# Kernel optimization log

Hardware: AMD Instinct MI355X
Metric: run time of the kernel (lower is better)

## Reference

```python
import jax, jax.numpy as jnp
import numpy as np

N = 50000   # nodes
E = 800000  # edges per edge type
H = 4       # attention heads
C = 64      # per-head out channels
EPS = 1e-5  # batchnorm eps


def gat_conv(x, ei, W, a_s, a_d, b):
    # PyG GATConv with add_self_loops=True, concat=True, negative_slope=0.2
    h = (x @ W).reshape(-1, H, C)                      # [N,H,C]
    sl = jnp.arange(N)
    src = jnp.concatenate([ei[0], sl])                 # [E+N]
    dst = jnp.concatenate([ei[1], sl])
    al_s = (h * a_s).sum(-1)                           # [N,H]
    al_d = (h * a_d).sum(-1)
    e = jax.nn.leaky_relu(al_s[src] + al_d[dst], 0.2)  # [E+N,H]
    m = jax.ops.segment_max(e, dst, num_segments=N)    # segment softmax over dst
    ex = jnp.exp(e - m[dst])
    s = jax.ops.segment_sum(ex, dst, num_segments=N)
    alpha = ex / (s[dst] + 1e-16)                      # [E+N,H]
    out = jax.ops.segment_sum(alpha[:, :, None] * h[src], dst, num_segments=N)
    return out.reshape(N, H * C) + b


def bn(x, g, b):
    mu = x.mean(0)
    v = jnp.var(x, 0)
    return g * (x - mu) * jax.lax.rsqrt(v + EPS) + b


def setup_inputs() -> dict:
    key = jax.random.key(0)
    ks = jax.random.split(key, 20)
    p = {}
    p["x"] = jax.random.normal(ks[0], (N, 128), jnp.float32)
    p["edge_index_spatial"] = jax.random.randint(ks[1], (2, E), 0, N)
    p["edge_index_temporal"] = jax.random.randint(ks[2], (2, E), 0, N)
    ins = [128, 256, 256, 256]
    k = 3
    for i in range(4):
        sc = 1.0 / np.sqrt(ins[i]).astype(np.float32)
        p[f"W{i+1}"] = jax.random.normal(ks[k], (ins[i], H * C), jnp.float32) * sc; k += 1
        p[f"as{i+1}"] = jax.random.normal(ks[k], (H, C), jnp.float32) * 0.1; k += 1
        p[f"ad{i+1}"] = jax.random.normal(ks[k], (H, C), jnp.float32) * 0.1; k += 1
        p[f"b{i+1}"] = jnp.zeros((H * C,), jnp.float32)
        p[f"g{i+1}"] = jnp.ones((H * C,), jnp.float32)
        p[f"be{i+1}"] = jnp.zeros((H * C,), jnp.float32)
    p["Wl"] = jax.random.normal(ks[k], (H * C, 32), jnp.float32) * (1.0 / 16.0)
    p["bl"] = jnp.zeros((32,), jnp.float32)
    return p


def reference(x, edge_index_spatial, edge_index_temporal,
              W1, as1, ad1, b1, g1, be1,
              W2, as2, ad2, b2, g2, be2,
              W3, as3, ad3, b3, g3, be3,
              W4, as4, ad4, b4, g4, be4,
              Wl, bl):
    h = jax.nn.relu(bn(gat_conv(x, edge_index_spatial, W1, as1, ad1, b1), g1, be1))
    h = jax.nn.relu(bn(gat_conv(h, edge_index_spatial, W2, as2, ad2, b2), g2, be2))
    h = jax.nn.relu(bn(gat_conv(h, edge_index_temporal, W3, as3, ad3, b3), g3, be3))
    h = jax.nn.relu(bn(gat_conv(h, edge_index_temporal, W4, as4, ad4, b4), g4, be4))
    return h @ Wl + bl
```

## Files before the change

### kernel.cpp

```cpp
#include <hip/hip_runtime.h>
#include <hip/hip_bf16.h>
#include <hip/hip_fp16.h>
#include <math.h>

#define N_NODES 50000
#define N_EDGES 800000
#define NH 4
#define HC 256
#define TOT_E (N_EDGES + N_NODES)
#define SCAN_NB ((N_NODES + 255) / 256)

static __device__ __forceinline__ float lrelu(float x) { return x >= 0.f ? x : 0.2f * x; }

__global__ __launch_bounds__(256) void count_kernel(const int* __restrict__ ei,
                                                    int* __restrict__ cnt) {
    int i = blockIdx.x * blockDim.x + threadIdx.x;
    if (i >= TOT_E) return;
    int dst = (i < N_EDGES) ? ei[N_EDGES + i] : (i - N_EDGES);
    atomicAdd(&cnt[dst], 1);
}

__global__ __launch_bounds__(256) void scan1_kernel(const int* __restrict__ cnt,
                                                    int* __restrict__ offs,
                                                    int* __restrict__ bsum) {
    __shared__ int sm[256];
    const int t = threadIdx.x;
    const int base = blockIdx.x * 256;
    int v = (base + t < N_NODES) ? cnt[base + t] : 0;
    sm[t] = v;
    __syncthreads();
#pragma unroll
    for (int d = 1; d < 256; d <<= 1) {
        int add = (t >= d) ? sm[t - d] : 0;
        __syncthreads();
        sm[t] += add;
        __syncthreads();
    }
    if (base + t < N_NODES) offs[base + t] = sm[t] - v;
    if (t == 255) bsum[blockIdx.x] = sm[255];
}

__global__ __launch_bounds__(256) void scan2_kernel(int* __restrict__ bsum,
                                                    int* __restrict__ total) {
    __shared__ int sm[256];
    const int t = threadIdx.x;
    int v = (t < SCAN_NB) ? bsum[t] : 0;
    sm[t] = v;
    __syncthreads();
#pragma unroll
    for (int d = 1; d < 256; d <<= 1) {
        int add = (t >= d) ? sm[t - d] : 0;
        __syncthreads();
        sm[t] += add;
        __syncthreads();
    }
    if (t < SCAN_NB) bsum[t] = sm[t] - v;
    if (t == 255) *total = sm[255];
}

__global__ __launch_bounds__(256) void scan3_kernel(int* __restrict__ offs,
                                                    const int* __restrict__ bsum) {
    int i = blockIdx.x * blockDim.x + threadIdx.x;
    if (i < N_NODES) offs[i] += bsum[i >> 8];
}

__global__ __launch_bounds__(256) void scatter_kernel(const int* __restrict__ ei,
                                                      const int* __restrict__ offs,
                                                      int* __restrict__ cursor,
                                                      int* __restrict__ ssrc) {
    int i = blockIdx.x * blockDim.x + threadIdx.x;
    if (i >= TOT_E) return;
    int src, dst;
    if (i < N_EDGES) { src = ei[i]; dst = ei[N_EDGES + i]; }
    else             { src = i - N_EDGES; dst = src; }
    int pos = offs[dst] + atomicAdd(&cursor[dst], 1);
    ssrc[pos] = src;
}

__global__ __launch_bounds__(256) void gemm_kernel(const float* __restrict__ A,
                                                   const float* __restrict__ B,
                                                   __half* __restrict__ C,
                                                   const float* __restrict__ bnscale,
                                                   const float* __restrict__ bnshift,
                                                   const float* __restrict__ a_s,
                                                   const float* __restrict__ a_d,
                                                   float* __restrict__ als,
                                                   float* __restrict__ ald,
                                                   int M, int K) {
    __shared__ float As[16][128];
    __shared__ float Bs[16][128];
    const int t = threadIdx.x;
    const int tx = t & 15, ty = t >> 4;
    const int bm = blockIdx.x * 128;
    const int bn = blockIdx.y * 128;
    const int ar = t >> 2;
    const int ak = (t & 3) << 2;
    const int bk = t >> 5;
    const int bn4 = (t & 31) << 2;
    float acc[8][8] = {{0.f}};
    for (int k0 = 0; k0 < K; k0 += 16) {
        float4 sc = make_float4(1.f, 1.f, 1.f, 1.f);
        float4 sh = make_float4(0.f, 0.f, 0.f, 0.f);
        if (bnscale) {
            sc = *(const float4*)(bnscale + k0 + ak);
            sh = *(const float4*)(bnshift + k0 + ak);
        }
#pragma unroll
        for (int r = 0; r < 2; ++r) {
            int row = bm + r * 64 + ar;
            float4 a4 = make_float4(0.f, 0.f, 0.f, 0.f);
            if (row < M) a4 = *(const float4*)(A + (size_t)row * K + k0 + ak);
            if (bnscale) {
                a4.x = fmaxf(0.f, fmaf(a4.x, sc.x, sh.x));
                a4.y = fmaxf(0.f, fmaf(a4.y, sc.y, sh.y));
                a4.z = fmaxf(0.f, fmaf(a4.z, sc.z, sh.z));
                a4.w = fmaxf(0.f, fmaf(a4.w, sc.w, sh.w));
            }
            As[ak + 0][r * 64 + ar] = a4.x;
            As[ak + 1][r * 64 + ar] = a4.y;
            As[ak + 2][r * 64 + ar] = a4.z;
            As[ak + 3][r * 64 + ar] = a4.w;
        }
#pragma unroll
        for (int r = 0; r < 2; ++r) {
            int kk = r * 8 + bk;
            *(float4*)&Bs[kk][bn4] = *(const float4*)(B + (size_t)(k0 + kk) * HC + bn + bn4);
        }
        __syncthreads();
#pragma unroll
        for (int kk = 0; kk < 16; ++kk) {
            float a[8], b[8];
            *(float4*)&a[0] = *(const float4*)&As[kk][ty * 8];
            *(float4*)&a[4] = *(const float4*)&As[kk][ty * 8 + 4];
            *(float4*)&b[0] = *(const float4*)&Bs[kk][tx * 8];
            *(float4*)&b[4] = *(const float4*)&Bs[kk][tx * 8 + 4];
#pragma unroll
            for (int i = 0; i < 8; ++i)
#pragma unroll
                for (int j = 0; j < 8; ++j)
                    acc[i][j] = fmaf(a[i], b[j], acc[i][j]);
        }
        __syncthreads();
    }
#pragma unroll
    for (int i = 0; i < 8; ++i) {
        int row = bm + ty * 8 + i;
        if (row < M) {
            __half hv[8];
#pragma unroll
            for (int j = 0; j < 8; ++j) hv[j] = __float2half(acc[i][j]);
            *(uint4*)(C + (size_t)row * HC + bn + tx * 8) = *(uint4*)hv;
        }
    }
    const int ch0 = bn + tx * 8;
    float asv[8], adv[8];
#pragma unroll
    for (int j = 0; j < 8; ++j) { asv[j] = a_s[ch0 + j]; adv[j] = a_d[ch0 + j]; }
#pragma unroll
    for (int i = 0; i < 8; ++i) {
        int row = bm + ty * 8 + i;
        float ps = 0.f, pd = 0.f;
#pragma unroll
        for (int j = 0; j < 8; ++j) {
            ps = fmaf(acc[i][j], asv[j], ps);
            pd = fmaf(acc[i][j], adv[j], pd);
        }
#pragma unroll
        for (int d = 1; d < 8; d <<= 1) {
            ps += __shfl_xor(ps, d, 64);
            pd += __shfl_xor(pd, d, 64);
        }
        if ((tx & 7) == 0 && row < M) {
            int head = (bn >> 6) + (tx >> 3);
            als[row * NH + head] = ps;
            ald[row * NH + head] = pd;
        }
    }
}

__global__ __launch_bounds__(256) void gat_edge_kernel(const __half* __restrict__ h,
                                                       const int* __restrict__ offs,
                                                       const int* __restrict__ ssrc,
                                                       const float* __restrict__ als,
                                                       const float* __restrict__ ald,
                                                       const float* __restrict__ bias,
                                                       float* __restrict__ out) {
    __shared__ float ex_sm[4][64][NH];
    __shared__ int   src_sm[4][64];
    const int lane = threadIdx.x & 63;
    const int w = threadIdx.x >> 6;
    const int v = (blockIdx.x << 2) + w;
    if (v >= N_NODES) return;
    const int hh = lane >> 4;
    const float4 aldv4 = *(const float4*)(ald + v * NH);
    const int beg = offs[v], end = offs[v + 1];

    float4 m4 = make_float4(-INFINITY, -INFINITY, -INFINITY, -INFINITY);
    float4 s4 = make_float4(0.f, 0.f, 0.f, 0.f);
    float ax = 0.f, ay = 0.f, az = 0.f, aw = 0.f;

    for (int c0 = beg; c0 < end; c0 += 64) {
        const int n = min(64, end - c0);
        const int s0 = ssrc[c0];
        int srcl = s0;
        float4 e4 = make_float4(-INFINITY, -INFINITY, -INFINITY, -INFINITY);
        if (lane < n) {
            srcl = ssrc[c0 + lane];
            float4 a4 = *(const float4*)(als + srcl * NH);
            e4.x = lrelu(a4.x + aldv4.x);
            e4.y = lrelu(a4.y + aldv4.y);
            e4.z = lrelu(a4.z + aldv4.z);
            e4.w = lrelu(a4.w + aldv4.w);
        }
        float4 cm = e4;
#pragma unroll
        for (int d = 1; d < 64; d <<= 1) {
            cm.x = fmaxf(cm.x, __shfl_xor(cm.x, d, 64));
            cm.y = fmaxf(cm.y, __shfl_xor(cm.y, d, 64));
            cm.z = fmaxf(cm.z, __shfl_xor(cm.z, d, 64));
            cm.w = fmaxf(cm.w, __shfl_xor(cm.w, d, 64));
        }
        const float4 mn = make_float4(fmaxf(m4.x, cm.x), fmaxf(m4.y, cm.y),
                                      fmaxf(m4.z, cm.z), fmaxf(m4.w, cm.w));
        const float4 r4 = make_float4(__expf(m4.x - mn.x), __expf(m4.y - mn.y),
                                      __expf(m4.z - mn.z), __expf(m4.w - mn.w));
        float4 ex4;
        ex4.x = __expf(e4.x - mn.x);
        ex4.y = __expf(e4.y - mn.y);
        ex4.z = __expf(e4.z - mn.z);
        ex4.w = __expf(e4.w - mn.w);
        src_sm[w][lane] = srcl;
        *(float4*)&ex_sm[w][lane][0] = ex4;
        float4 se = ex4;
#pragma unroll
        for (int d = 1; d < 64; d <<= 1) {
            se.x += __shfl_xor(se.x, d, 64);
            se.y += __shfl_xor(se.y, d, 64);
            se.z += __shfl_xor(se.z, d, 64);
            se.w += __shfl_xor(se.w, d, 64);
        }
        s4 = make_float4(fmaf(s4.x, r4.x, se.x), fmaf(s4.y, r4.y, se.y),
                         fmaf(s4.z, r4.z, se.z), fmaf(s4.w, r4.w, se.w));
        const float rh = hh == 0 ? r4.x : hh == 1 ? r4.y : hh == 2 ? r4.z : r4.w;
        ax *= rh; ay *= rh; az *= rh; aw *= rh;
        m4 = mn;

        const int trip = (n + 7) & ~7;
        int sj[8]; float wj[8];
#pragma unroll
        for (int q = 0; q < 8; ++q) { sj[q] = src_sm[w][q]; wj[q] = ex_sm[w][q][hh]; }
        const int co = lane << 2;
        for (int j = 0; j < trip; j += 8) {
            uint2 raw[8];
#pragma unroll
            for (int q = 0; q < 8; ++q)
                raw[q] = *(const uint2*)(h + (size_t)sj[q] * HC + co);
            float u[8];
#pragma unroll
            for (int q = 0; q < 8; ++q) u[q] = wj[q];
            if (j + 8 < trip) {
#pragma unroll
                for (int q = 0; q < 8; ++q) {
                    sj[q] = src_sm[w][j + 8 + q];
                    wj[q] = ex_sm[w][j + 8 + q][hh];
                }
            }
#pragma unroll
            for (int q = 0; q < 8; ++q) {
                const __half2 lo = *reinterpret_cast<const __half2*>(&raw[q].x);
                const __half2 hi = *reinterpret_cast<const __half2*>(&raw[q].y);
                const float2 f0 = __half22float2(lo);
                const float2 f1 = __half22float2(hi);
                ax = fmaf(u[q], f0.x, ax); ay = fmaf(u[q], f0.y, ay);
                az = fmaf(u[q], f1.x, az); aw = fmaf(u[q], f1.y, aw);
            }
        }
    }

    const float sh = hh == 0 ? s4.x : hh == 1 ? s4.y : hh == 2 ? s4.z : s4.w;
    const float inv = 1.f / (sh + 1e-16f);
    const float4 b4 = *(const float4*)(bias + (lane << 2));
    *(float4*)(out + (size_t)v * HC + (lane << 2)) =
        make_float4(fmaf(ax, inv, b4.x), fmaf(ay, inv, b4.y),
                    fmaf(az, inv, b4.z), fmaf(aw, inv, b4.w));
}

__global__ __launch_bounds__(256) void bn_stats_kernel(const float* __restrict__ y,
                                                       double* __restrict__ sum,
                                                       double* __restrict__ sqsum) {
    const int t = threadIdx.x;
    const int r0 = blockIdx.x * 128;
    const int r1 = min(r0 + 128, N_NODES);
    float s = 0.f, q = 0.f;
    for (int r = r0; r < r1; ++r) {
        float v = y[(size_t)r * HC + t];
        s += v;
        q = fmaf(v, v, q);
    }
    atomicAdd(&sum[t], (double)s);
    atomicAdd(&sqsum[t], (double)q);
}

__global__ void bn_finalize_kernel(const double* __restrict__ sum,
                                   const double* __restrict__ sqsum,
                                   const float* __restrict__ g,
                                   const float* __restrict__ be,
                                   float* __restrict__ scale,
                                   float* __restrict__ shift) {
    int t = threadIdx.x;
    double mean = sum[t] / (double)N_NODES;
    double var = sqsum[t] / (double)N_NODES - mean * mean;
    float sc = g[t] * rsqrtf((float)var + 1e-5f);
    scale[t] = sc;
    shift[t] = be[t] - (float)mean * sc;
}

__global__ __launch_bounds__(256) void linear_kernel(const float* __restrict__ y,
                                                     const float* __restrict__ Wl,
                                                     const float* __restrict__ bl,
                                                     const float* __restrict__ scale,
                                                     const float* __restrict__ shift,
                                                     float* __restrict__ out) {
    __shared__ float Wls[256 * 32];
    __shared__ float scs[256], shs[256];
    const int t = threadIdx.x;
    for (int i = t; i < 256 * 32; i += 256) Wls[i] = Wl[i];
    scs[t] = scale[t];
    shs[t] = shift[t];
    __syncthreads();
    int gid = blockIdx.x * 256 + t;
    if (gid >= N_NODES * 32) return;
    int n = gid >> 5, j = gid & 31;
    float acc = bl[j];
    const float4* yrow = (const float4*)(y + (size_t)n * HC);
#pragma unroll
    for (int k4 = 0; k4 < 64; ++k4) {
        float4 y4 = yrow[k4];
        int k = k4 << 2;
        y4.x = fmaxf(0.f, fmaf(y4.x, scs[k + 0], shs[k + 0]));
        y4.y = fmaxf(0.f, fmaf(y4.y, scs[k + 1], shs[k + 1]));
        y4.z = fmaxf(0.f, fmaf(y4.z, scs[k + 2], shs[k + 2]));
        y4.w = fmaxf(0.f, fmaf(y4.w, scs[k + 3], shs[k + 3]));
        acc = fmaf(y4.x, Wls[(k + 0) * 32 + j], acc);
        acc = fmaf(y4.y, Wls[(k + 1) * 32 + j], acc);
        acc = fmaf(y4.z, Wls[(k + 2) * 32 + j], acc);
        acc = fmaf(y4.w, Wls[(k + 3) * 32 + j], acc);
    }
    out[gid] = acc;
}

extern "C" void kernel_launch(void* const* d_in, const int* in_sizes, int n_in,
                              void* d_out, int out_size, void* d_ws, size_t ws_size,
                              hipStream_t stream) {
    const float* x     = (const float*)d_in[0];
    const int* ei_sp   = (const int*)d_in[1];
    const int* ei_tp   = (const int*)d_in[2];
    const float* Wl    = (const float*)d_in[27];
    const float* bl    = (const float*)d_in[28];

    char* ws = (char*)d_ws;
    size_t off = 0;
    auto alloc = [&](size_t bytes) -> char* {
        char* p = ws + off;
        off = (off + bytes + 255) & ~(size_t)255;
        return p;
    };
    __half* buf0   = (__half*)alloc((size_t)N_NODES * HC * 2);
    float* buf1    = (float*)alloc((size_t)N_NODES * HC * 4);
    float* als     = (float*)alloc((size_t)N_NODES * NH * 4);
    float* ald     = (float*)alloc((size_t)N_NODES * NH * 4);
    int*   offs_sp = (int*)alloc((size_t)(N_NODES + 1) * 4);
    int*   offs_tp = (int*)alloc((size_t)(N_NODES + 1) * 4);
    int*   src_sp  = (int*)alloc((size_t)TOT_E * 4);
    int*   src_tp  = (int*)alloc((size_t)TOT_E * 4);
    int*   cnt     = (int*)alloc((size_t)N_NODES * 4);
    int*   bsum    = (int*)alloc((size_t)SCAN_NB * 4);
    double* bnsum  = (double*)alloc(256 * 8 * 2);
    double* bnsq   = bnsum + 256;
    float* scale   = (float*)alloc(256 * 4);
    float* shift   = (float*)alloc(256 * 4);
    (void)ws_size; (void)in_sizes; (void)n_in; (void)out_size;

    const int EB = (TOT_E + 255) / 256;

    hipMemsetAsync(cnt, 0, (size_t)N_NODES * 4, stream);
    count_kernel<<<EB, 256, 0, stream>>>(ei_sp, cnt);
    scan1_kernel<<<SCAN_NB, 256, 0, stream>>>(cnt, offs_sp, bsum);
    scan2_kernel<<<1, 256, 0, stream>>>(bsum, offs_sp + N_NODES);
    scan3_kernel<<<SCAN_NB, 256, 0, stream>>>(offs_sp, bsum);
    hipMemsetAsync(cnt, 0, (size_t)N_NODES * 4, stream);
    scatter_kernel<<<EB, 256, 0, stream>>>(ei_sp, offs_sp, cnt, src_sp);

    hipMemsetAsync(cnt, 0, (size_t)N_NODES * 4, stream);
    count_kernel<<<EB, 256, 0, stream>>>(ei_tp, cnt);
    scan1_kernel<<<SCAN_NB, 256, 0, stream>>>(cnt, offs_tp, bsum);
    scan2_kernel<<<1, 256, 0, stream>>>(bsum, offs_tp + N_NODES);
    scan3_kernel<<<SCAN_NB, 256, 0, stream>>>(offs_tp, bsum);
    hipMemsetAsync(cnt, 0, (size_t)N_NODES * 4, stream);
    scatter_kernel<<<EB, 256, 0, stream>>>(ei_tp, offs_tp, cnt, src_tp);

    const int NB4 = (N_NODES + 3) / 4;
    const dim3 ggrid((N_NODES + 127) / 128, 2);
    for (int L = 0; L < 4; ++L) {
        const float* in = (L == 0) ? x : buf1;
        const int K = (L == 0) ? 128 : 256;
        const float* bns = (L == 0) ? nullptr : scale;
        const float* bnh = (L == 0) ? nullptr : shift;
        const int* offs = (L < 2) ? offs_sp : offs_tp;
        const int* ssrc = (L < 2) ? src_sp : src_tp;
        const int base = 3 + L * 6;
        const float* W  = (const float*)d_in[base + 0];
        const float* as_ = (const float*)d_in[base + 1];
        const float* ad_ = (const float*)d_in[base + 2];
        const float* b_  = (const float*)d_in[base + 3];
        const float* g_  = (const float*)d_in[base + 4];
        const float* be_ = (const float*)d_in[base + 5];

        gemm_kernel<<<ggrid, 256, 0, stream>>>(in, W, buf0, bns, bnh,
                                               as_, ad_, als, ald, N_NODES, K);
        gat_edge_kernel<<<NB4, 256, 0, stream>>>(buf0, offs, ssrc, als, ald, b_, buf1);

        hipMemsetAsync(bnsum, 0, 256 * 8 * 2, stream);
        bn_stats_kernel<<<(N_NODES + 127) / 128, 256, 0, stream>>>(buf1, bnsum, bnsq);
        bn_finalize_kernel<<<1, 256, 0, stream>>>(bnsum, bnsq, g_, be_, scale, shift);
    }

    linear_kernel<<<(N_NODES * 32 + 255) / 256, 256, 0, stream>>>(buf1, Wl, bl,
                                                                  scale, shift,
                                                                  (float*)d_out);
}
```

Before: 1.178 ms.

## Use split-bf16 MFMA matrix cores for the node feature GEMM

Replaces the FP32 scalar-FMA tiled GEMM with an MFMA 16x16x32 bf16 implementation. Each fp32 input is split into high and low bf16 parts, and three MFMAs per tile (hi*hi, hi*lo, lo*hi) recover near-fp32 accuracy. The shared-memory layout changes to k-contiguous bf16 tiles, and the attention-logit epilogue is reworked for the MFMA output layout. This adds conversion work and makes the fp16 output stores scalar and strided in exchange for much higher matrix throughput.

```diff
diff --git a/kernel.cpp b/kernel.cpp
--- a/kernel.cpp
+++ b/kernel.cpp
@@ -10,7 +10,16 @@
 #define TOT_E (N_EDGES + N_NODES)
 #define SCAN_NB ((N_NODES + 255) / 256)
 
+typedef __attribute__((ext_vector_type(8))) short short8;
+typedef __attribute__((ext_vector_type(4))) float f32x4;
+
 static __device__ __forceinline__ float lrelu(float x) { return x >= 0.f ? x : 0.2f * x; }
+
+static __device__ __forceinline__ unsigned short bf16_rne(float x) {
+    unsigned int u = __float_as_uint(x);
+    u += 0x7fff + ((u >> 16) & 1);
+    return (unsigned short)(u >> 16);
+}
 
 __global__ __launch_bounds__(256) void count_kernel(const int* __restrict__ ei,
                                                     int* __restrict__ cnt) {
@@ -87,93 +96,135 @@
                                                    float* __restrict__ als,
                                                    float* __restrict__ ald,
                                                    int M, int K) {
-    __shared__ float As[16][128];
-    __shared__ float Bs[16][128];
+    __shared__ unsigned short Ah[128][40], Al[128][40];
+    __shared__ unsigned short Bh[128][40], Bl[128][40];
     const int t = threadIdx.x;
-    const int tx = t & 15, ty = t >> 4;
+    const int l = t & 63;
+    const int w = t >> 6;
+    const int wr = w >> 1, wc = w & 1;
+    const int fr = l & 15;
+    const int kg = (l >> 4) << 3;
     const int bm = blockIdx.x * 128;
     const int bn = blockIdx.y * 128;
-    const int ar = t >> 2;
-    const int ak = (t & 3) << 2;
-    const int bk = t >> 5;
-    const int bn4 = (t & 31) << 2;
-    float acc[8][8] = {{0.f}};
-    for (int k0 = 0; k0 < K; k0 += 16) {
-        float4 sc = make_float4(1.f, 1.f, 1.f, 1.f);
-        float4 sh = make_float4(0.f, 0.f, 0.f, 0.f);
-        if (bnscale) {
-            sc = *(const float4*)(bnscale + k0 + ak);
-            sh = *(const float4*)(bnshift + k0 + ak);
-        }
-#pragma unroll
-        for (int r = 0; r < 2; ++r) {
-            int row = bm + r * 64 + ar;
-            float4 a4 = make_float4(0.f, 0.f, 0.f, 0.f);
-            if (row < M) a4 = *(const float4*)(A + (size_t)row * K + k0 + ak);
-            if (bnscale) {
-                a4.x = fmaxf(0.f, fmaf(a4.x, sc.x, sh.x));
-                a4.y = fmaxf(0.f, fmaf(a4.y, sc.y, sh.y));
-                a4.z = fmaxf(0.f, fmaf(a4.z, sc.z, sh.z));
-                a4.w = fmaxf(0.f, fmaf(a4.w, sc.w, sh.w));
-            }
-            As[ak + 0][r * 64 + ar] = a4.x;
-            As[ak + 1][r * 64 + ar] = a4.y;
-            As[ak + 2][r * 64 + ar] = a4.z;
-            As[ak + 3][r * 64 + ar] = a4.w;
-        }
-#pragma unroll
-        for (int r = 0; r < 2; ++r) {
-            int kk = r * 8 + bk;
-            *(float4*)&Bs[kk][bn4] = *(const float4*)(B + (size_t)(k0 + kk) * HC + bn + bn4);
-        }
-        __syncthreads();
-#pragma unroll
-        for (int kk = 0; kk < 16; ++kk) {
-            float a[8], b[8];
-            *(float4*)&a[0] = *(const float4*)&As[kk][ty * 8];
-            *(float4*)&a[4] = *(const float4*)&As[kk][ty * 8 + 4];
-            *(float4*)&b[0] = *(const float4*)&Bs[kk][tx * 8];
-            *(float4*)&b[4] = *(const float4*)&Bs[kk][tx * 8 + 4];
-#pragma unroll
-            for (int i = 0; i < 8; ++i)
-#pragma unroll
-                for (int j = 0; j < 8; ++j)
-                    acc[i][j] = fmaf(a[i], b[j], acc[i][j]);
-        }
-        __syncthreads();
-    }
-#pragma unroll
-    for (int i = 0; i < 8; ++i) {
-        int row = bm + ty * 8 + i;
-        if (row < M) {
-            __half hv[8];
-#pragma unroll
-            for (int j = 0; j < 8; ++j) hv[j] = __float2half(acc[i][j]);
-            *(uint4*)(C + (size_t)row * HC + bn + tx * 8) = *(uint4*)hv;
-        }
-    }
-    const int ch0 = bn + tx * 8;
-    float asv[8], adv[8];
-#pragma unroll
-    for (int j = 0; j < 8; ++j) { asv[j] = a_s[ch0 + j]; adv[j] = a_d[ch0 + j]; }
-#pragma unroll
-    for (int i = 0; i < 8; ++i) {
-        int row = bm + ty * 8 + i;
-        float ps = 0.f, pd = 0.f;
-#pragma unroll
-        for (int j = 0; j < 8; ++j) {
-            ps = fmaf(acc[i][j], asv[j], ps);
-            pd = fmaf(acc[i][j], adv[j], pd);
-        }
-#pragma unroll
-        for (int d = 1; d < 8; d <<= 1) {
-            ps += __shfl_xor(ps, d, 64);
-            pd += __shfl_xor(pd, d, 64);
-        }
-        if ((tx & 7) == 0 && row < M) {
-            int head = (bn >> 6) + (tx >> 3);
-            als[row * NH + head] = ps;
-            ald[row * NH + head] = pd;
+    const int ra = t >> 1, ka = (t & 1) << 4;
+    const int nb = (t & 31) << 2, kb = (t >> 5) << 2;
+
+    f32x4 acc[4][4] = {};
+
+    for (int k0 = 0; k0 < K; k0 += 32) {
+        {
+            const int row = bm + ra;
+#pragma unroll
+            for (int i = 0; i < 4; ++i) {
+                const int kk = ka + 4 * i;
+                float4 a4 = make_float4(0.f, 0.f, 0.f, 0.f);
+                if (row < M) a4 = *(const float4*)(A + (size_t)row * K + k0 + kk);
+                if (bnscale) {
+                    float4 sc = *(const float4*)(bnscale + k0 + kk);
+                    float4 sh = *(const float4*)(bnshift + k0 + kk);
+                    a4.x = fmaxf(0.f, fmaf(a4.x, sc.x, sh.x));
+                    a4.y = fmaxf(0.f, fmaf(a4.y, sc.y, sh.y));
+                    a4.z = fmaxf(0.f, fmaf(a4.z, sc.z, sh.z));
+                    a4.w = fmaxf(0.f, fmaf(a4.w, sc.w, sh.w));
+                }
+                unsigned short h[4], lo[4];
+                float v[4] = {a4.x, a4.y, a4.z, a4.w};
+#pragma unroll
+                for (int q = 0; q < 4; ++q) {
+                    h[q] = bf16_rne(v[q]);
+                    float hf = __uint_as_float((unsigned int)h[q] << 16);
+                    lo[q] = bf16_rne(v[q] - hf);
+                }
+                *(uint2*)&Ah[ra][kk] = *(uint2*)h;
+                *(uint2*)&Al[ra][kk] = *(uint2*)lo;
+            }
+        }
+        {
+            float4 bv[4];
+#pragma unroll
+            for (int i = 0; i < 4; ++i)
+                bv[i] = *(const float4*)(B + (size_t)(k0 + kb + i) * HC + bn + nb);
+#pragma unroll
+            for (int c = 0; c < 4; ++c) {
+                float v[4] = {c == 0 ? bv[0].x : c == 1 ? bv[0].y : c == 2 ? bv[0].z : bv[0].w,
+                              c == 0 ? bv[1].x : c == 1 ? bv[1].y : c == 2 ? bv[1].z : bv[1].w,
+                              c == 0 ? bv[2].x : c == 1 ? bv[2].y : c == 2 ? bv[2].z : bv[2].w,
+                              c == 0 ? bv[3].x : c == 1 ? bv[3].y : c == 2 ? bv[3].z : bv[3].w};
+                unsigned short h[4], lo[4];
+#pragma unroll
+                for (int q = 0; q < 4; ++q) {
+                    h[q] = bf16_rne(v[q]);
+                    float hf = __uint_as_float((unsigned int)h[q] << 16);
+                    lo[q] = bf16_rne(v[q] - hf);
+                }
+                *(uint2*)&Bh[nb + c][kb] = *(uint2*)h;
+                *(uint2*)&Bl[nb + c][kb] = *(uint2*)lo;
+            }
+        }
+        __syncthreads();
+        short8 ahf[4], alf[4], bhf[4], blf[4];
+#pragma unroll
+        for (int m = 0; m < 4; ++m) {
+            ahf[m] = *(const short8*)&Ah[wr * 64 + m * 16 + fr][kg];
+            alf[m] = *(const short8*)&Al[wr * 64 + m * 16 + fr][kg];
+        }
+#pragma unroll
+        for (int n = 0; n < 4; ++n) {
+            bhf[n] = *(const short8*)&Bh[wc * 64 + n * 16 + fr][kg];
+            blf[n] = *(const short8*)&Bl[wc * 64 + n * 16 + fr][kg];
+        }
+#pragma unroll
+        for (int m = 0; m < 4; ++m)
+#pragma unroll
+            for (int n = 0; n < 4; ++n) {
+                acc[m][n] = __builtin_amdgcn_mfma_f32_16x16x32_bf16(ahf[m], bhf[n], acc[m][n], 0, 0, 0);
+                acc[m][n] = __builtin_amdgcn_mfma_f32_16x16x32_bf16(ahf[m], blf[n], acc[m][n], 0, 0, 0);
+                acc[m][n] = __builtin_amdgcn_mfma_f32_16x16x32_bf16(alf[m], bhf[n], acc[m][n], 0, 0, 0);
+            }
+        __syncthreads();
+    }
+
+#pragma unroll
+    for (int m = 0; m < 4; ++m) {
+        const int row0 = bm + wr * 64 + m * 16 + ((l >> 4) << 2);
+#pragma unroll
+        for (int n = 0; n < 4; ++n) {
+            const int col = bn + wc * 64 + n * 16 + fr;
+#pragma unroll
+            for (int r = 0; r < 4; ++r) {
+                if (row0 + r < M)
+                    C[(size_t)(row0 + r) * HC + col] = __float2half(acc[m][n][r]);
+            }
+        }
+    }
+    const int hw = (bn >> 6) + wc;
+    float asv[4], adv[4];
+#pragma unroll
+    for (int n = 0; n < 4; ++n) {
+        const int col = bn + wc * 64 + n * 16 + fr;
+        asv[n] = a_s[col];
+        adv[n] = a_d[col];
+    }
+#pragma unroll
+    for (int m = 0; m < 4; ++m) {
+        const int row0 = bm + wr * 64 + m * 16 + ((l >> 4) << 2);
+#pragma unroll
+        for (int r = 0; r < 4; ++r) {
+            float ps = 0.f, pd = 0.f;
+#pragma unroll
+            for (int n = 0; n < 4; ++n) {
+                ps = fmaf(acc[m][n][r], asv[n], ps);
+                pd = fmaf(acc[m][n][r], adv[n], pd);
+            }
+#pragma unroll
+            for (int d = 1; d < 16; d <<= 1) {
+                ps += __shfl_xor(ps, d, 64);
+                pd += __shfl_xor(pd, d, 64);
+            }
+            if (fr == 0 && row0 + r < M) {
+                als[(row0 + r) * NH + hw] = ps;
+                ald[(row0 + r) * NH + hw] = pd;
+            }
         }
     }
 }
```

Result: faster. 1.057 ms (-10.2%).
